# Performance work log

Measured on AMD Instinct MI355X. Metric: run time of the kernel, lower is better.

Reference implementation:

```python
import jax, jax.numpy as jnp
import numpy as np

QMIN, QMAX = -128, 127  # signed int8 range


def setup_inputs() -> dict:
    key = jax.random.key(0)
    k_x, k_w, k_b = jax.random.split(key, 3)
    N, C_in, H, W = 32, 128, 56, 56
    C_out, kH, kW = 256, 3, 3
    # int8-valued tensors carried as int32 (jax-friendly); values in [-128, 127]
    x = jax.random.randint(k_x, (N, C_in, H, W), 0, 256, dtype=jnp.int32) - 128
    weight = jax.random.randint(k_w, (C_out, C_in, kH, kW), 0, 256, dtype=jnp.int32) - 128
    # int32 bias, already quantized with scale s_in * s_w
    bias = jax.random.randint(k_b, (C_out,), -(2 ** 14), 2 ** 14, dtype=jnp.int32)
    return {
        "x": x,
        "weight": weight,
        "bias": bias,
        "input_scale": jnp.float32(0.02),
        "weight_scale": jnp.float32(0.005),
        "output_scale": jnp.float32(0.05),
        "input_zero_point": jnp.int32(-5),
        "output_zero_point": jnp.int32(3),
    }


def reference(x, weight, bias, input_scale, weight_scale, output_scale,
              input_zero_point, output_zero_point):
    # Dequant-style integer conv: shift input by its zero point (weights are
    # symmetric, zero point 0), accumulate in fp32 (stands in for int32 acc).
    x_f = (x - input_zero_point).astype(jnp.float32)
    w_f = weight.astype(jnp.float32)
    acc = jax.lax.conv_general_dilated(
        x_f, w_f,
        window_strides=(1, 1),
        padding=((1, 1), (1, 1)),
        dimension_numbers=("NCHW", "OIHW", "NCHW"),
    )
    acc = acc + bias.astype(jnp.float32)[None, :, None, None]
    # Requantize: scale fusion + output zero point, round, clamp to int8.
    requant_scale = input_scale * weight_scale / output_scale
    y = acc * requant_scale + output_zero_point.astype(jnp.float32)
    y_q = jnp.clip(jnp.round(y), QMIN, QMAX).astype(jnp.int8)
    return y_q
```

## Files before the change

### kernel.cpp

```cpp
#include <hip/hip_runtime.h>
#include <stdint.h>


#define NB 32
#define CI 128
#define HH 56
#define WW 56
#define CO 256
#define SPA (HH * WW)
#define HP 58
#define WP 64
#define XP2_BYTES (NB * HP * WP * CI)
#define BP_BYTES (9 * 2 * 4 * CO * 16)
#define ABUF (4 * 8192)

typedef int v4i __attribute__((ext_vector_type(4)));

__global__ __launch_bounds__(256) void prep_kernel(
    const int* __restrict__ x, const int* __restrict__ wgt,
    const int* __restrict__ bias, const int* __restrict__ zpi,
    int8_t* __restrict__ xp2, int8_t* __restrict__ bp, int* __restrict__ BG)
{
    __shared__ int sm[1824];
    const int tid = threadIdx.x, bid = blockIdx.x;
    const int zp = *zpi;
    const int zp4 = (zp & 255) * 0x01010101;

    if (bid < HH * NB) {
        const int n = bid / HH, h = bid % HH;
        #pragma unroll
        for (int it = 0; it < 7; ++it) {
            int j = tid + it * 256;
            int ci = j / 14, w4 = j - ci * 14;
            const v4i v = *(const v4i*)(x + ((n * CI + ci) * HH + h) * WW + w4 * 4);
            sm[w4 * 130 + ci] = (v.x & 255) | ((v.y & 255) << 8) |
                                ((v.z & 255) << 16) | (v.w << 24);
        }
        __syncthreads();
        int* od = (int*)xp2 + (n * HP + h + 1) * (WP * CI / 4);
        #pragma unroll
        for (int it = 0; it < 8; ++it) {
            int j = tid + it * 256;
            int widx = j >> 5, ci4 = j & 31;
            int val = zp4;
            if (widx >= 1 && widx <= WW) {
                int w = widx - 1;
                int base = (w >> 2) * 130 + ci4 * 4;
                int sh = (w & 3) * 8;
                val = ((sm[base] >> sh) & 0xff) | (((sm[base+1] >> sh) & 0xff) << 8) |
                      (((sm[base+2] >> sh) & 0xff) << 16) | ((sm[base+3] >> sh) << 24);
            }
            od[j ^ ((widx & 7) << 2)] = val;
        }
    } else if (bid < HH * NB + 2 * NB) {
        const int z = bid - HH * NB;
        const int n = z >> 1, hidx = (z & 1) ? (HP - 1) : 0;
        int* od = (int*)xp2 + (n * HP + hidx) * (WP * CI / 4);
        #pragma unroll
        for (int it = 0; it < 8; ++it) od[tid + it * 256] = zp4;
    } else {
        const int co = bid - (HH * NB + 2 * NB);
        for (int j = tid; j < 1152; j += 256) sm[j] = wgt[co * 1152 + j];
        __syncthreads();
        for (int j = tid; j < 288; j += 256) {
            int j4 = j & 3, q = (j >> 2) & 3, c64 = (j >> 4) & 1, t = j >> 5;
            int ci = c64 * 64 + q * 16 + j4 * 4;
            int b0 = sm[(ci + 0) * 9 + t] & 255, b1 = sm[(ci + 1) * 9 + t] & 255;
            int b2 = sm[(ci + 2) * 9 + t] & 255, b3 = sm[(ci + 3) * 9 + t];
            ((int*)bp)[((t * 2 + c64) * 4 + q) * 1024 + co * 4 + j4] =
                b0 | (b1 << 8) | (b2 << 16) | (b3 << 24);
        }
        if (tid < 9) {
            int s = 0;
            for (int ci = 0; ci < CI; ++ci) s += sm[ci * 9 + tid];
            sm[1152 + tid] = s;
        }
        __syncthreads();
        if (tid == 0) {
            int s9 = 0;
            for (int t = 0; t < 9; ++t) s9 += sm[1152 + t];
            BG[co] = bias[co] - zp * s9;
        }
    }
}

__global__ __launch_bounds__(256, 2) void qconv_mfma(
    const int8_t* __restrict__ xp2, const int8_t* __restrict__ bp,
    const int* __restrict__ BG,
    const float* __restrict__ si, const float* __restrict__ sw,
    const float* __restrict__ so, const int* __restrict__ zpo,
    int* __restrict__ out)
{
    const int tid  = threadIdx.x, lane = tid & 63, wid = tid >> 6;
    const int quad = lane >> 4, lo16 = lane & 15;
    const int bid  = blockIdx.x;
    const int x    = bid & 7, r = bid >> 3;
    const int n    = x * 4 + (r & 3);
    const int co64 = (r >> 2) & 3;
    const int g    = r >> 4;
    const int cw   = co64 * 64 + wid * 16;

    __shared__ __attribute__((aligned(16))) int8_t Asm[2][ABUF];

    const int8_t* src0 = xp2 + (((size_t)n * HP + 2 * g) << 13);
    #pragma unroll
    for (int k = 0; k < 8; ++k) {
        const int u = wid + 4 * k;
        __builtin_amdgcn_global_load_lds(
            (const __attribute__((address_space(1))) void*)(src0 + (u << 10) + lane * 16),
            (__attribute__((address_space(3))) void*)(&Asm[0][u << 10]), 16, 0, 0);
    }

    v4i breg[9][2];
    #pragma unroll
    for (int t = 0; t < 9; ++t)
        #pragma unroll
        for (int c = 0; c < 2; ++c)
            breg[t][c] = *(const v4i*)(bp + (((t * 2 + c) * 4 + quad) << 12) +
                                       (cw + lo16) * 16);

    const int bg0 = BG[cw + lo16];
    const float rs = (*si) * (*sw) / (*so);
    const float zo = (float)(*zpo);

    int rowoff[7], colp[7][3];
    #pragma unroll
    for (int mt = 0; mt < 7; ++mt) {
        const int ml = mt * 16 + lo16;
        const int srow = ml / 56, scol = ml - srow * 56;
        rowoff[mt] = srow * 8192;
        #pragma unroll
        for (int dc = 0; dc < 3; ++dc) {
            const int c2 = scol + dc;
            colp[mt][dc] = (c2 * 128 + quad * 16) ^ ((c2 & 7) << 4);
        }
    }

    int* optr = out + ((size_t)n * CO + cw + lo16) * SPA + quad * 4;

    __syncthreads();

    #pragma unroll 1
    for (int t7 = 0; t7 < 7; ++t7) {
        const int s = g + 4 * t7;
        const int8_t* curA = Asm[t7 & 1];

        if (t7 < 6) {
            const int8_t* srcn = xp2 + (((size_t)n * HP + 2 * (s + 4)) << 13);
            int8_t* dst = (int8_t*)Asm[(t7 & 1) ^ 1];
            #pragma unroll
            for (int k = 0; k < 8; ++k) {
                const int u = wid + 4 * k;
                __builtin_amdgcn_global_load_lds(
                    (const __attribute__((address_space(1))) void*)(srcn + (u << 10) + lane * 16),
                    (__attribute__((address_space(3))) void*)(dst + (u << 10)), 16, 0, 0);
            }
        }
        __builtin_amdgcn_sched_barrier(0);

        v4i acc[7];
        #pragma unroll
        for (int mt = 0; mt < 7; ++mt) acc[mt] = (v4i){0, 0, 0, 0};

        #pragma unroll
        for (int tp = 0; tp < 9; ++tp) {
            const int dr = tp / 3, dc = tp % 3;
            #pragma unroll
            for (int mt = 0; mt < 7; ++mt) {
                const int off = rowoff[mt] + dr * 8192 + colp[mt][dc];
                v4i a0 = *(const v4i*)(curA + off);
                v4i a1 = *(const v4i*)(curA + (off ^ 64));
                acc[mt] = __builtin_amdgcn_mfma_i32_16x16x64_i8(a0, breg[tp][0], acc[mt], 0, 0, 0);
                acc[mt] = __builtin_amdgcn_mfma_i32_16x16x64_i8(a1, breg[tp][1], acc[mt], 0, 0, 0);
            }
        }

        const int m0 = s * 112;
        #pragma unroll
        for (int mt = 0; mt < 7; ++mt) {
            v4i vv;
            #pragma unroll
            for (int i = 0; i < 4; ++i) {
                float yv = rintf((float)(acc[mt][i] + bg0) * rs + zo);
                yv = fminf(fmaxf(yv, -128.f), 127.f);
                vv[i] = (int)yv;
            }
            *(v4i*)(optr + m0 + mt * 16) = vv;
        }

        if (t7 < 6) {
            __builtin_amdgcn_sched_barrier(0);
            asm volatile("s_waitcnt vmcnt(7)" ::: "memory");
            __builtin_amdgcn_s_barrier();
            __builtin_amdgcn_sched_barrier(0);
        }
    }
}

extern "C" void kernel_launch(void* const* d_in, const int* in_sizes, int n_in,
                              void* d_out, int out_size, void* d_ws, size_t ws_size,
                              hipStream_t stream) {
    const int*   x    = (const int*)d_in[0];
    const int*   wgt  = (const int*)d_in[1];
    const int*   bias = (const int*)d_in[2];
    const float* si   = (const float*)d_in[3];
    const float* sw   = (const float*)d_in[4];
    const float* so   = (const float*)d_in[5];
    const int*   zpi  = (const int*)d_in[6];
    const int*   zpo  = (const int*)d_in[7];
    int* out = (int*)d_out;

    int8_t* xp2 = (int8_t*)d_ws;
    int8_t* bp  = xp2 + XP2_BYTES;
    int*    bg  = (int*)(bp + BP_BYTES);

    prep_kernel<<<HH * NB + 2 * NB + CO, 256, 0, stream>>>(x, wgt, bias, zpi, xp2, bp, bg);
    qconv_mfma<<<512, 256, 0, stream>>>(xp2, bp, bg, si, sw, so, zpo, out);
}
```

Measured before the change: 180.7 us.

## Widen per-wave output channels to 32 and halve blocks per image row group

Each wave now computes two 16-channel output tiles from the same LDS A fragments, so every LDS read feeds two MFMAs, and each block covers 128 channels instead of 64. The spatial tile schedule moves from 4 groups of 7 tiles to 8 groups of 3 or 4 tiles, which leaves the 512-block grid unchanged but gives blocks uneven work. It also packs the swizzle offsets into fewer registers, raises wave priority around the MFMA loop, and adjusts the vmcnt wait for the doubled stores. The cost is roughly double the B-register footprint and accumulators, which raises VGPR pressure at launch_bounds(256,2).

After: 224.9 us. +24.4%, slower.

```diff
diff --git a/kernel.cpp b/kernel.cpp
--- a/kernel.cpp
+++ b/kernel.cpp
@@ -94,15 +94,16 @@
     const int tid  = threadIdx.x, lane = tid & 63, wid = tid >> 6;
     const int quad = lane >> 4, lo16 = lane & 15;
     const int bid  = blockIdx.x;
-    const int x    = bid & 7, r = bid >> 3;
-    const int n    = x * 4 + (r & 3);
-    const int co64 = (r >> 2) & 3;
-    const int g    = r >> 4;
-    const int cw   = co64 * 64 + wid * 16;
+    const int xcd  = bid & 7, i = bid >> 3;
+    const int n    = xcd * 4 + (i & 3);
+    const int cb   = (i >> 2) & 1;
+    const int sA   = i >> 3;
+    const int ntiles = (i < 32) ? 4 : 3;
+    const int cw   = cb * 128 + wid * 32;
 
     __shared__ __attribute__((aligned(16))) int8_t Asm[2][ABUF];
 
-    const int8_t* src0 = xp2 + (((size_t)n * HP + 2 * g) << 13);
+    const int8_t* src0 = xp2 + (((size_t)n * HP + 2 * sA) << 13);
     #pragma unroll
     for (int k = 0; k < 8; ++k) {
         const int u = wid + 4 * k;
@@ -111,43 +112,48 @@
             (__attribute__((address_space(3))) void*)(&Asm[0][u << 10]), 16, 0, 0);
     }
 
-    v4i breg[9][2];
+    v4i breg[9][2][2];
     #pragma unroll
     for (int t = 0; t < 9; ++t)
         #pragma unroll
         for (int c = 0; c < 2; ++c)
-            breg[t][c] = *(const v4i*)(bp + (((t * 2 + c) * 4 + quad) << 12) +
-                                       (cw + lo16) * 16);
-
-    const int bg0 = BG[cw + lo16];
+            #pragma unroll
+            for (int ct = 0; ct < 2; ++ct) {
+                breg[t][c][ct] = *(const v4i*)(bp + (((t * 2 + c) * 4 + quad) << 12) +
+                                               ((cw + ct * 16 + lo16) << 4));
+                asm volatile("" : "+v"(breg[t][c][ct]));
+            }
+
+    int bgv[2];
+    #pragma unroll
+    for (int ct = 0; ct < 2; ++ct) bgv[ct] = BG[cw + ct * 16 + lo16];
     const float rs = (*si) * (*sw) / (*so);
     const float zo = (float)(*zpo);
 
-    int rowoff[7], colp[7][3];
+    int boff[7], sw3[7];
     #pragma unroll
     for (int mt = 0; mt < 7; ++mt) {
         const int ml = mt * 16 + lo16;
         const int srow = ml / 56, scol = ml - srow * 56;
-        rowoff[mt] = srow * 8192;
-        #pragma unroll
-        for (int dc = 0; dc < 3; ++dc) {
-            const int c2 = scol + dc;
-            colp[mt][dc] = (c2 * 128 + quad * 16) ^ ((c2 & 7) << 4);
-        }
-    }
-
-    int* optr = out + ((size_t)n * CO + cw + lo16) * SPA + quad * 4;
+        boff[mt] = srow * 8192 + scol * 128 + quad * 16;
+        int s0 = ((scol + 0) & 7) << 4, s1 = ((scol + 1) & 7) << 4,
+            s2 = ((scol + 2) & 7) << 4;
+        sw3[mt] = s0 | (s1 << 8) | (s2 << 16);
+    }
+
+    int* optr0 = out + ((size_t)n * CO + cw + lo16) * SPA + quad * 4;
+    int* optr1 = optr0 + 16 * SPA;
 
     __syncthreads();
 
     #pragma unroll 1
-    for (int t7 = 0; t7 < 7; ++t7) {
-        const int s = g + 4 * t7;
-        const int8_t* curA = Asm[t7 & 1];
-
-        if (t7 < 6) {
-            const int8_t* srcn = xp2 + (((size_t)n * HP + 2 * (s + 4)) << 13);
-            int8_t* dst = (int8_t*)Asm[(t7 & 1) ^ 1];
+    for (int j = 0; j < ntiles; ++j) {
+        const int s = sA + 8 * j;
+        const int8_t* curA = Asm[j & 1];
+
+        if (j + 1 < ntiles) {
+            const int8_t* srcn = xp2 + (((size_t)n * HP + 2 * (s + 8)) << 13);
+            int8_t* dst = (int8_t*)Asm[(j & 1) ^ 1];
             #pragma unroll
             for (int k = 0; k < 8; ++k) {
                 const int u = wid + 4 * k;
@@ -158,39 +164,49 @@
         }
         __builtin_amdgcn_sched_barrier(0);
 
-        v4i acc[7];
-        #pragma unroll
-        for (int mt = 0; mt < 7; ++mt) acc[mt] = (v4i){0, 0, 0, 0};
-
+        v4i acc[7][2];
+        #pragma unroll
+        for (int mt = 0; mt < 7; ++mt) {
+            acc[mt][0] = (v4i){0, 0, 0, 0};
+            acc[mt][1] = (v4i){0, 0, 0, 0};
+        }
+
+        __builtin_amdgcn_s_setprio(1);
         #pragma unroll
         for (int tp = 0; tp < 9; ++tp) {
             const int dr = tp / 3, dc = tp % 3;
             #pragma unroll
             for (int mt = 0; mt < 7; ++mt) {
-                const int off = rowoff[mt] + dr * 8192 + colp[mt][dc];
-                v4i a0 = *(const v4i*)(curA + off);
-                v4i a1 = *(const v4i*)(curA + (off ^ 64));
-                acc[mt] = __builtin_amdgcn_mfma_i32_16x16x64_i8(a0, breg[tp][0], acc[mt], 0, 0, 0);
-                acc[mt] = __builtin_amdgcn_mfma_i32_16x16x64_i8(a1, breg[tp][1], acc[mt], 0, 0, 0);
-            }
-        }
+                const int off  = boff[mt] + dr * 8192 + dc * 128;
+                const int phys = off ^ ((sw3[mt] >> (8 * dc)) & 0x70);
+                v4i a0 = *(const v4i*)(curA + phys);
+                v4i a1 = *(const v4i*)(curA + (phys ^ 64));
+                acc[mt][0] = __builtin_amdgcn_mfma_i32_16x16x64_i8(a0, breg[tp][0][0], acc[mt][0], 0, 0, 0);
+                acc[mt][1] = __builtin_amdgcn_mfma_i32_16x16x64_i8(a0, breg[tp][0][1], acc[mt][1], 0, 0, 0);
+                acc[mt][0] = __builtin_amdgcn_mfma_i32_16x16x64_i8(a1, breg[tp][1][0], acc[mt][0], 0, 0, 0);
+                acc[mt][1] = __builtin_amdgcn_mfma_i32_16x16x64_i8(a1, breg[tp][1][1], acc[mt][1], 0, 0, 0);
+            }
+        }
+        __builtin_amdgcn_s_setprio(0);
 
         const int m0 = s * 112;
         #pragma unroll
         for (int mt = 0; mt < 7; ++mt) {
-            v4i vv;
-            #pragma unroll
-            for (int i = 0; i < 4; ++i) {
-                float yv = rintf((float)(acc[mt][i] + bg0) * rs + zo);
-                yv = fminf(fmaxf(yv, -128.f), 127.f);
-                vv[i] = (int)yv;
-            }
-            *(v4i*)(optr + m0 + mt * 16) = vv;
-        }
-
-        if (t7 < 6) {
+            v4i v0, v1;
+            #pragma unroll
+            for (int i4 = 0; i4 < 4; ++i4) {
+                float y0 = rintf((float)(acc[mt][0][i4] + bgv[0]) * rs + zo);
+                float y1 = rintf((float)(acc[mt][1][i4] + bgv[1]) * rs + zo);
+                v0[i4] = (int)fminf(fmaxf(y0, -128.f), 127.f);
+                v1[i4] = (int)fminf(fmaxf(y1, -128.f), 127.f);
+            }
+            *(v4i*)(optr0 + m0 + mt * 16) = v0;
+            *(v4i*)(optr1 + m0 + mt * 16) = v1;
+        }
+
+        if (j + 1 < ntiles) {
             __builtin_amdgcn_sched_barrier(0);
-            asm volatile("s_waitcnt vmcnt(7)" ::: "memory");
+            asm volatile("s_waitcnt vmcnt(14)" ::: "memory");
             __builtin_amdgcn_s_barrier();
             __builtin_amdgcn_sched_barrier(0);
         }
```
